# Performance work log

Measured on AMD Instinct MI355X. Metric: run time of the kernel, lower is better.

Reference implementation:

```python
import jax, jax.numpy as jnp
import numpy as np

B, N, C, NPOINT, NSAMPLE, NHEAD, NLAYERS, DOUT = 8, 4096, 128, 1024, 32, 4, 2, 256
EPS = 1e-5


def setup_inputs() -> dict:
    key = jax.random.key(0)
    ks = jax.random.split(key, 12)
    rn = lambda k, s: jax.random.normal(k, s, jnp.float32) * 0.05
    return {
        "xyz": jax.random.normal(ks[0], (B, 3, N), jnp.float32),
        "features": jax.random.normal(ks[1], (B, C, N), jnp.float32),
        # position-encoding MLP (1x1 convs) + BatchNorm2d (inference, running mean=0 var=1)
        "pe_w1": rn(ks[2], (C // 2, 3)), "pe_b1": jnp.zeros((C // 2,), jnp.float32),
        "bn_g": jnp.ones((C // 2,), jnp.float32), "bn_b": jnp.zeros((C // 2,), jnp.float32),
        "pe_w2": rn(ks[3], (C, C // 2)), "pe_b2": jnp.zeros((C,), jnp.float32),
        # 2 pre-norm transformer encoder layers (stacked params)
        "in_w": rn(ks[4], (NLAYERS, 3 * C, C)), "in_b": jnp.zeros((NLAYERS, 3 * C), jnp.float32),
        "out_w": rn(ks[5], (NLAYERS, C, C)), "out_b": jnp.zeros((NLAYERS, C), jnp.float32),
        "ln1_g": jnp.ones((NLAYERS, C), jnp.float32), "ln1_b": jnp.zeros((NLAYERS, C), jnp.float32),
        "ln2_g": jnp.ones((NLAYERS, C), jnp.float32), "ln2_b": jnp.zeros((NLAYERS, C), jnp.float32),
        "ff1_w": rn(ks[6], (NLAYERS, 2 * C, C)), "ff1_b": jnp.zeros((NLAYERS, 2 * C), jnp.float32),
        "ff2_w": rn(ks[7], (NLAYERS, C, 2 * C)), "ff2_b": jnp.zeros((NLAYERS, C), jnp.float32),
        # final 1x1 conv (fc)
        "fc_w": rn(ks[8], (DOUT, C)), "fc_b": jnp.zeros((DOUT,), jnp.float32),
    }


def _fps(pts, npoint):
    # pts: [B, N, 3]; iterative farthest point sampling (start at index 0)
    b, n, _ = pts.shape
    d0 = jnp.full((b, n), 1e10, pts.dtype)
    f0 = jnp.zeros((b,), jnp.int32)

    def step(carry, _):
        dist, far = carry
        c = jnp.take_along_axis(pts, far[:, None, None], axis=1)  # [B,1,3]
        d = jnp.sum((pts - c) ** 2, axis=-1)                      # [B,N]
        dist = jnp.minimum(dist, d)
        return (dist, jnp.argmax(dist, axis=-1).astype(jnp.int32)), far

    _, idx = jax.lax.scan(step, (d0, f0), None, length=npoint)
    return idx.T  # [B, npoint]


def _knn(nsample, pts, queries):
    # pts [B,N,3], queries [B,S,3] -> [B,S,nsample] nearest-neighbor indices
    sqd = (jnp.sum(queries ** 2, -1)[:, :, None] + jnp.sum(pts ** 2, -1)[:, None, :]
           - 2.0 * jnp.einsum('bsc,bnc->bsn', queries, pts))
    _, idx = jax.lax.top_k(-sqd, nsample)
    return idx


_gather = jax.vmap(lambda p, i: p[i])  # per-batch fancy gather


def _ln(x, g, b):
    m = jnp.mean(x, -1, keepdims=True)
    v = jnp.var(x, -1, keepdims=True)
    return (x - m) * jax.lax.rsqrt(v + EPS) * g + b


def _forward(xyz, features, pe_w1, pe_b1, bn_g, bn_b, pe_w2, pe_b2,
             in_w, in_b, out_w, out_b, ln1_g, ln1_b, ln2_g, ln2_b,
             ff1_w, ff1_b, ff2_w, ff2_b, fc_w, fc_b):
    xyz_t = xyz.transpose(0, 2, 1)                      # [B,N,3]
    fps_idx = _fps(xyz_t, NPOINT)                       # [B,S]
    new_xyz = _gather(xyz_t, fps_idx)                   # [B,S,3]
    gidx = _knn(NSAMPLE, xyz_t, new_xyz)                # [B,S,ns]
    gxyz = _gather(xyz_t, gidx)                         # [B,S,ns,3]
    gfeat = _gather(features.transpose(0, 2, 1), gidx)  # [B,S,ns,C]

    # position encoding: 1x1 conv MLP, BN in inference mode (mean=0, var=1)
    h = gxyz @ pe_w1.T + pe_b1
    h = h / jnp.sqrt(jnp.float32(1.0 + EPS)) * bn_g + bn_b
    pe = jax.nn.relu(h) @ pe_w2.T + pe_b2               # [B,S,ns,C]

    x = (gfeat + pe).reshape(B * NPOINT, NSAMPLE, C)    # groups as batch, seq=ns
    hd = C // NHEAD
    scale = 1.0 / jnp.sqrt(jnp.float32(hd))
    for l in range(NLAYERS):
        hN = _ln(x, ln1_g[l], ln1_b[l])
        qkv = hN @ in_w[l].T + in_b[l]
        q, k, v = jnp.split(qkv, 3, axis=-1)
        q = q.reshape(-1, NSAMPLE, NHEAD, hd)
        k = k.reshape(-1, NSAMPLE, NHEAD, hd)
        v = v.reshape(-1, NSAMPLE, NHEAD, hd)
        att = jax.nn.softmax(jnp.einsum('mqhd,mkhd->mhqk', q, k) * scale, axis=-1)
        a = jnp.einsum('mhqk,mkhd->mqhd', att, v).reshape(-1, NSAMPLE, C)
        x = x + (a @ out_w[l].T + out_b[l])
        h2 = _ln(x, ln2_g[l], ln2_b[l])
        x = x + (jax.nn.relu(h2 @ ff1_w[l].T + ff1_b[l]) @ ff2_w[l].T + ff2_b[l])

    pooled = x.reshape(B, NPOINT, NSAMPLE, C).max(axis=2)  # maxpool over neighbors
    out = pooled @ fc_w.T + fc_b                           # [B,S,DOUT]
    return new_xyz.transpose(0, 2, 1), out.transpose(0, 2, 1)


def reference(xyz, features, pe_w1, pe_b1, bn_g, bn_b, pe_w2, pe_b2,
              in_w, in_b, out_w, out_b, ln1_g, ln1_b, ln2_g, ln2_b,
              ff1_w, ff1_b, ff2_w, ff2_b, fc_w, fc_b):
    return _forward(xyz, features, pe_w1, pe_b1, bn_g, bn_b, pe_w2, pe_b2,
                    in_w, in_b, out_w, out_b, ln1_g, ln1_b, ln2_g, ln2_b,
                    ff1_w, ff1_b, ff2_w, ff2_b, fc_w, fc_b)
```

## Files before the change

### kernel.cpp

```cpp
#include <hip/hip_runtime.h>

typedef unsigned int u32;
typedef unsigned long long u64;
typedef unsigned short u16;
typedef __attribute__((ext_vector_type(8))) short bf16x8;
typedef __attribute__((ext_vector_type(4))) float f32x4;

#define DEV __device__ __forceinline__

DEV float sq3(float x, float y, float z) {
#pragma clang fp contract(off)
  return (x * x + y * y) + z * z;
}
DEV float knn_sqd(float4 Q, float4 p) {
#pragma clang fp contract(off)
  float dot = (Q.x * p.x + Q.y * p.y) + Q.z * p.z;
  return (Q.w + p.w) - 2.0f * dot;
}
DEV float dot4(float4 a, float4 b) {
  return (a.x * b.x + a.y * b.y) + (a.z * b.z + a.w * b.w);
}
DEV u32 f2bfu(float f) {
  u32 u = __float_as_uint(f);
  return (u + 0x7fffu + ((u >> 16) & 1u)) >> 16;
}
DEV f32x4 MFMA(bf16x8 a, bf16x8 b, f32x4 c) {
  return __builtin_amdgcn_mfma_f32_16x16x32_bf16(a, b, c, 0, 0, 0);
}

enum : int {
  W_PEW1 = 0, W_PEB1 = 192, W_BNG = 256, W_BNB = 320,
  W_PEW2 = 384, W_PEB2 = 8576,
  W_INW  = 8704,   W_INB  = 107008,
  W_OUTW = 107776, W_OUTB = 140544,
  W_LN1G = 140800, W_LN1B = 141056, W_LN2G = 141312, W_LN2B = 141568,
  W_FF1W = 141824, W_FF1B = 207360,
  W_FF2W = 207872, W_FF2B = 273408,
  W_FCW  = 273664, W_FCB  = 306432,
  W_TOTAL = 306688
};
enum : int { WP_QB = 0, WP_FB = 768, WP_TOTAL = 1280 };
enum : int {
  WB_Q  = 0,
  WB_O  = 98304,
  WB_F1 = 131072,
  WB_F2 = 196608,
  WB_P2 = 262144,
  WB_TOTAL = 270336
};

static const size_t OFF_XYZW  = 1226752;
static const size_t OFF_NEWX  = 1751040;
static const size_t OFF_KNN   = 1882112;
static const size_t OFF_WP    = 2930688;
static const size_t OFF_WB    = 2936064;
static const size_t OFF_FEATT = 3476736;
static const size_t END_BIG   = 20253952;

struct WArgs { const float* p[20]; };

__global__ void k_setup(WArgs a, float* __restrict__ wf, float* __restrict__ wp,
                        u16* __restrict__ wb, const float* __restrict__ xyz,
                        float4* __restrict__ xyzw) {
  const int blk = blockIdx.x, tid = threadIdx.x;
  if (blk < 1198) {
    const int idx = blk * 256 + tid;
    if (idx >= W_TOTAL) return;
    const int sz[20] = {192, 64, 64, 64, 8192, 128, 98304, 768, 32768, 256,
                        256, 256, 256, 256, 65536, 512, 65536, 256, 32768, 256};
    int rem = idx;
#pragma unroll
    for (int s = 0; s < 20; ++s) {
      if (rem < sz[s]) { wf[idx] = a.p[s][rem]; return; }
      rem -= sz[s];
    }
    return;
  }
  if (blk < 1206) {
    const int idx = (blk - 1198) * 256 + tid;
    if (idx >= 1920) return;
    if (idx < 768) {
      const int l = idx / 384, o = idx % 384;
      const float* W = a.p[6] + l * 49152 + o * 128;
      const float* G = a.p[10] + l * 128;
      const float* Bl = a.p[11] + l * 128;
      float acc = a.p[7][l * 384 + o];
      u16* ph = wb + WB_Q + (l * 384 + o) * 128;
      for (int c = 0; c < 128; ++c) {
        const float w = W[c];
        acc += Bl[c] * w;
        ph[c] = (u16)f2bfu(w * G[c]);
      }
      wp[WP_QB + l * 384 + o] = acc;
    } else if (idx < 1280) {
      const int j2 = idx - 768, l = j2 / 256, o = j2 % 256;
      const float* W = a.p[14] + l * 32768 + o * 128;
      const float* G = a.p[12] + l * 128;
      const float* Bl = a.p[13] + l * 128;
      float acc = a.p[15][l * 256 + o];
      u16* ph = wb + WB_F1 + (l * 256 + o) * 128;
      for (int c = 0; c < 128; ++c) {
        const float w = W[c];
        acc += Bl[c] * w;
        ph[c] = (u16)f2bfu(w * G[c]);
      }
      wp[WP_FB + l * 256 + o] = acc;
    } else if (idx < 1536) {
      const int j2 = idx - 1280, l = j2 / 128, o = j2 % 128;
      const float* W = a.p[8] + l * 16384 + o * 128;
      u16* ph = wb + WB_O + (l * 128 + o) * 128;
      for (int c = 0; c < 128; ++c) ph[c] = (u16)f2bfu(W[c]);
    } else if (idx < 1792) {
      const int j2 = idx - 1536, l = j2 / 128, o = j2 % 128;
      const float* W = a.p[16] + l * 32768 + o * 256;
      u16* ph = wb + WB_F2 + (l * 128 + o) * 256;
      for (int c = 0; c < 256; ++c) ph[c] = (u16)f2bfu(W[c]);
    } else {
      const int o = idx - 1792;
      const float* W = a.p[4] + o * 64;
      u16* ph = wb + WB_P2 + o * 64;
      for (int c = 0; c < 64; ++c) ph[c] = (u16)f2bfu(W[c]);
    }
    return;
  }
  {
    const int i = (blk - 1206) * 256 + tid;
    const int b = i >> 12, n = i & 4095;
    const size_t s = (size_t)b * 12288 + n;
    float x = xyz[s], y = xyz[s + 4096], z = xyz[s + 8192];
    xyzw[i] = make_float4(x, y, z, sq3(x, y, z));
  }
}

__global__ __launch_bounds__(256, 1) void k_pre(
    const float4* __restrict__ xyzw, float4* __restrict__ new_xyzw,
    float* __restrict__ out_xyz, const float* __restrict__ feat,
    float* __restrict__ featT) {
  __shared__ float PXs[4096], PYs[4096], PZs[4096];
  __shared__ u64 wkk[2][4];
  __shared__ float tile[32][33];
  const int tid = threadIdx.x;
  if (blockIdx.x >= 8) {
    const int bb = blockIdx.x - 8;
    const int b = bb >> 9, r2 = bb & 511;
    const int n0 = (r2 >> 2) << 5, c0 = (r2 & 3) << 5;
    const int tx = tid & 31, ty = tid >> 5;
#pragma unroll
    for (int i = 0; i < 4; ++i) {
      const int c = c0 + ty + (i << 3);
      tile[ty + (i << 3)][tx] =
          __builtin_nontemporal_load(&feat[(size_t)b * 524288 + (size_t)c * 4096 + n0 + tx]);
    }
    __syncthreads();
#pragma unroll
    for (int i = 0; i < 4; ++i) {
      const int n = n0 + ty + (i << 3);
      __builtin_nontemporal_store(tile[tx][ty + (i << 3)],
          &featT[(size_t)b * 524288 + (size_t)n * 128 + c0 + tx]);
    }
    return;
  }
  const int b = blockIdx.x;
  const float4* src = xyzw + (size_t)b * 4096;
  float px[16], py[16], pz[16], dm[16];
#pragma unroll
  for (int j = 0; j < 16; ++j) {
    float4 v = src[tid * 16 + j];
    PXs[tid * 16 + j] = v.x; PYs[tid * 16 + j] = v.y; PZs[tid * 16 + j] = v.z;
    px[j] = v.x; py[j] = v.y; pz[j] = v.z; dm[j] = 1e10f;
  }
  __syncthreads();
  float cx = PXs[0], cy = PYs[0], cz = PZs[0];
  if (tid == 0) {
    new_xyzw[(size_t)b * 1024] = make_float4(cx, cy, cz, sq3(cx, cy, cz));
    out_xyz[b * 3072]        = cx;
    out_xyz[b * 3072 + 1024] = cy;
    out_xyz[b * 3072 + 2048] = cz;
  }
  for (int t = 1; t < 1024; ++t) {
    {
      float dx = px[0] - cx, dy = py[0] - cy, dz = pz[0] - cz;
      dm[0] = fminf(dm[0], sq3(dx, dy, dz));
    }
    float bv = dm[0];
    int bi = tid * 16;
#pragma unroll
    for (int j = 1; j < 16; ++j) {
      float dx = px[j] - cx, dy = py[j] - cy, dz = pz[j] - cz;
      float d = sq3(dx, dy, dz);
      dm[j] = fminf(dm[j], d);
      if (dm[j] > bv) { bv = dm[j]; bi = tid * 16 + j; }
    }
    float mx = bv;
    mx = fmaxf(mx, __shfl_xor(mx, 1));
    mx = fmaxf(mx, __shfl_xor(mx, 2));
    mx = fmaxf(mx, __shfl_xor(mx, 4));
    mx = fmaxf(mx, __shfl_xor(mx, 8));
    mx = fmaxf(mx, __shfl_xor(mx, 16));
    mx = fmaxf(mx, __shfl_xor(mx, 32));
    const u64 ball = __ballot(bv == mx);
    const int wl2 = (int)(__ffsll((unsigned long long)ball) - 1);
    const int wbi = __shfl(bi, wl2);
    if ((tid & 63) == 0)
      wkk[t & 1][tid >> 6] = ((u64)__float_as_uint(mx) << 12) | (u32)(4095 - wbi);
    __syncthreads();
    const u64* wk = wkk[t & 1];
    u64 ka = wk[0] > wk[1] ? wk[0] : wk[1];
    u64 kb2 = wk[2] > wk[3] ? wk[2] : wk[3];
    u64 key = ka > kb2 ? ka : kb2;
    const int win = 4095 - (int)(key & 0xfffu);
    cx = PXs[win]; cy = PYs[win]; cz = PZs[win];
    if (tid == 0) {
      new_xyzw[(size_t)b * 1024 + t] = make_float4(cx, cy, cz, sq3(cx, cy, cz));
      out_xyz[b * 3072 + t]        = cx;
      out_xyz[b * 3072 + 1024 + t] = cy;
      out_xyz[b * 3072 + 2048 + t] = cz;
    }
  }
}

__global__ __launch_bounds__(128, 1) void k_knn(
    const float4* __restrict__ xyzw, const float4* __restrict__ qxyzw,
    int* __restrict__ knn) {
  __shared__ u64 LL[32 * 128];
  __shared__ int HH[4][32];
  const int tid = threadIdx.x;
  const int ql = tid >> 5, ss = tid & 31;
  const int b = blockIdx.x >> 8;
  const int q = ((blockIdx.x & 255) << 2) + ql;
  const float4 Q = qxyzw[(size_t)b * 1024 + q];
  u64 L[32];
#pragma unroll
  for (int i = 0; i < 32; ++i) L[i] = ~0ULL;
  const float4* P = xyzw + (size_t)b * 4096;
#pragma unroll 2
  for (int j = 0; j < 128; ++j) {
    const int n = j * 32 + ss;
    float4 p = P[n];
    float sqd = knn_sqd(Q, p);
    u32 u = __float_as_uint(sqd);
    u ^= (u32)((int)u >> 31) | 0x80000000u;
    const u64 key = ((u64)u << 12) | (u32)n;
    if (key < L[31]) {
#pragma unroll
      for (int i = 31; i >= 1; --i) {
        const u64 lo = L[i] < key ? L[i] : key;
        L[i] = lo > L[i - 1] ? lo : L[i - 1];
      }
      L[0] = L[0] < key ? L[0] : key;
    }
  }
#pragma unroll
  for (int i = 0; i < 32; ++i) LL[i * 128 + tid] = L[i];
  __syncthreads();
  if (ss == 0) {
#pragma unroll
    for (int t2 = 0; t2 < 32; ++t2) HH[ql][t2] = 0;
    const size_t ob = ((size_t)b * 1024 + q) * 32;
    for (int o = 0; o < 32; ++o) {
      u64 best = ~0ULL;
      int bs = 0;
#pragma unroll
      for (int t2 = 0; t2 < 32; ++t2) {
        const int hh = HH[ql][t2];
        const u64 v = (hh < 32) ? LL[hh * 128 + (ql * 32 + t2)] : ~0ULL;
        if (v < best) { best = v; bs = t2; }
      }
      HH[ql][bs]++;
      knn[ob + o] = (int)(best & 0xfffu);
    }
  }
}


DEV void ln_z(const float* __restrict__ X, u16* __restrict__ ZH, int tid) {
  const int r = tid >> 3, sub = tid & 7;
  const int xm = (r & 7) << 2;
  const float* row = X + r * 128;
  float4 v[4];
  float s = 0.f;
#pragma unroll
  for (int j = 0; j < 4; ++j) {
    v[j] = *(const float4*)&row[(sub * 16 + j * 4) ^ xm];
    s += (v[j].x + v[j].y) + (v[j].z + v[j].w);
  }
  s += __shfl_xor(s, 1); s += __shfl_xor(s, 2); s += __shfl_xor(s, 4);
  const float m = s * 0.0078125f;
  float qv = 0.f;
#pragma unroll
  for (int j = 0; j < 4; ++j) {
    float a = v[j].x - m, b = v[j].y - m, c = v[j].z - m, d = v[j].w - m;
    qv += (a * a + b * b) + (c * c + d * d);
  }
  qv += __shfl_xor(qv, 1); qv += __shfl_xor(qv, 2); qv += __shfl_xor(qv, 4);
  const float rstd = 1.0f / sqrtf(qv * 0.0078125f + 1e-5f);
  const int mask = (r & 7) << 3;
  float z[16];
#pragma unroll
  for (int j = 0; j < 4; ++j) {
    z[j * 4]     = (v[j].x - m) * rstd;
    z[j * 4 + 1] = (v[j].y - m) * rstd;
    z[j * 4 + 2] = (v[j].z - m) * rstd;
    z[j * 4 + 3] = (v[j].w - m) * rstd;
  }
#pragma unroll
  for (int i = 0; i < 8; ++i) {
    const u32 w = f2bfu(z[2 * i]) | (f2bfu(z[2 * i + 1]) << 16);
    *(u32*)&ZH[r * 128 + ((sub * 16 + 2 * i) ^ mask)] = w;
  }
}

template <int K, int AINS, int MODE>
DEV void gemmT(const u16* __restrict__ A, const u16* __restrict__ wbp,
               const float* __restrict__ bias, float* __restrict__ X,
               u16* __restrict__ OUTp, int co, int tid) {
  const int wv = tid >> 6, wl = tid & 63;
  const int c0 = wv * 32;
  const int lm = wl & 15, kb = wl >> 4;
  const int amask = (lm & 7) << 3;
  constexpr int KS = K / 32;
  constexpr int CH = (KS > 4) ? 4 : KS;
  f32x4 acc[2][2];
#pragma unroll
  for (int m = 0; m < 2; ++m)
#pragma unroll
    for (int t = 0; t < 2; ++t) acc[m][t] = (f32x4){0.f, 0.f, 0.f, 0.f};
#pragma unroll
  for (int kc = 0; kc < KS / CH; ++kc) {
    bf16x8 bfr[CH][2];
#pragma unroll
    for (int ks = 0; ks < CH; ++ks) {
      const int k0 = (kc * CH + ks) * 32 + kb * 8;
#pragma unroll
      for (int t = 0; t < 2; ++t)
        bfr[ks][t] = *(const bf16x8*)&wbp[(size_t)(c0 + t * 16 + lm) * K + k0];
    }
#pragma unroll
    for (int ks = 0; ks < CH; ++ks) {
      const int k0 = (kc * CH + ks) * 32 + kb * 8;
      const bf16x8 a0 = *(const bf16x8*)&A[(size_t)lm * AINS + (k0 ^ amask)];
      const bf16x8 a1 = *(const bf16x8*)&A[(size_t)(16 + lm) * AINS + (k0 ^ amask)];
#pragma unroll
      for (int t = 0; t < 2; ++t) {
        acc[0][t] = MFMA(a0, bfr[ks][t], acc[0][t]);
        acc[1][t] = MFMA(a1, bfr[ks][t], acc[1][t]);
      }
    }
  }
#pragma unroll
  for (int m = 0; m < 2; ++m)
#pragma unroll
    for (int t = 0; t < 2; ++t) {
      const int col = c0 + t * 16 + lm;
      const float bv = bias[col];
      if (MODE == 3) {
        const int j0 = m * 16 + kb * 4;
        const int base = (col & 31) * 256 + 128 + ((col >> 5) << 5) +
                         (j0 ^ ((col & 3) << 3));
        *(u32*)&OUTp[base]     = f2bfu(acc[m][t][0] + bv) | (f2bfu(acc[m][t][1] + bv) << 16);
        *(u32*)&OUTp[base + 2] = f2bfu(acc[m][t][2] + bv) | (f2bfu(acc[m][t][3] + bv) << 16);
      } else if (MODE == 1) {
#pragma unroll
        for (int j = 0; j < 4; ++j) {
          const int row = m * 16 + kb * 4 + j;
          X[row * 128 + (col ^ ((row & 7) << 2))] += acc[m][t][j] + bv;
        }
      } else {
#pragma unroll
        for (int j = 0; j < 4; ++j) {
          const int row = m * 16 + kb * 4 + j;
          float val = acc[m][t][j] + bv;
          if (MODE == 2) val = fmaxf(val, 0.f);
          OUTp[row * 256 + ((co + col) ^ ((row & 7) << 3))] = (u16)f2bfu(val);
        }
      }
    }
}

__global__ __launch_bounds__(256, 2) void k_xform(
    const float* __restrict__ feat, const float* __restrict__ featT, const int useT,
    const float4* __restrict__ xyzw, const int* __restrict__ knn,
    const float* __restrict__ wf, const float* __restrict__ wp,
    const u16* __restrict__ wb, float* __restrict__ out) {
  __shared__ __align__(16) float sm[10240];
  float* X  = sm;
  u16* ZH   = (u16*)(sm + 4096);
  u16* QKp  = (u16*)(sm + 6144);
  const int g = blockIdx.x, b = g >> 10, tid = threadIdx.x;
  const int r = tid >> 3, sub = tid & 7, cs = sub * 16;
  const int xm = (r & 7) << 2;
  const int n = knn[g * 32 + r];
  if (useT) {
    const f32x4* srcp = (const f32x4*)(featT + ((size_t)(b * 4096 + n)) * 128 + cs);
    float* dst = &X[r * 128];
#pragma unroll
    for (int j = 0; j < 4; ++j)
      *(f32x4*)&dst[(cs + j * 4) ^ xm] = __builtin_nontemporal_load(&srcp[j]);
  } else {
    const size_t fb0 = (size_t)b * 524288 + n;
    float* dst = &X[r * 128];
#pragma unroll
    for (int j = 0; j < 16; ++j)
      dst[(cs + j) ^ xm] = __builtin_nontemporal_load(&feat[fb0 + (size_t)(cs + j) * 4096]);
  }
  {
    const float4 g4 = xyzw[(size_t)b * 4096 + n];
    const float rs = 1.0f / sqrtf(1.0f + 1e-5f);
    const int mask = (r & 7) << 3;
#pragma unroll
    for (int i = 0; i < 4; ++i) {
      u32 wpk = 0;
#pragma unroll
      for (int e = 0; e < 2; ++e) {
        const int c = sub * 8 + 2 * i + e;
        float hv = g4.x * wf[W_PEW1 + c * 3] + g4.y * wf[W_PEW1 + c * 3 + 1] +
                   g4.z * wf[W_PEW1 + c * 3 + 2] + wf[W_PEB1 + c];
        hv = hv * (wf[W_BNG + c] * rs) + wf[W_BNB + c];
        hv = fmaxf(hv, 0.f);
        wpk |= f2bfu(hv) << (16 * e);
      }
      *(u32*)&ZH[r * 128 + ((sub * 8 + 2 * i) ^ mask)] = wpk;
    }
  }
  __syncthreads();
  gemmT<64, 128, 1>(ZH, wb + WB_P2, wf + W_PEB2, X, QKp, 0, tid);
  __syncthreads();
#pragma unroll 1
  for (int l = 0; l < 2; ++l) {
    ln_z(X, ZH, tid);
    __syncthreads();
    gemmT<128, 128, 0>(ZH, wb + WB_Q + l * 49152, wp + WP_QB + l * 384,
                       X, QKp, 0, tid);
    gemmT<128, 128, 0>(ZH, wb + WB_Q + l * 49152 + 16384,
                       wp + WP_QB + l * 384 + 128, X, QKp, 128, tid);
    __syncthreads();
    {
      const int wv = tid >> 6, wl = tid & 63;
      const int hh = wv, lm = wl & 15, kb = wl >> 4;
      bf16x8 qf[2], kf[2];
#pragma unroll
      for (int t = 0; t < 2; ++t) {
        const int rr = t * 16 + lm;
        const int msk = (rr & 7) << 3;
        qf[t] = *(const bf16x8*)&QKp[rr * 256 + ((hh * 32 + kb * 8) ^ msk)];
        kf[t] = *(const bf16x8*)&QKp[rr * 256 + ((128 + hh * 32 + kb * 8) ^ msk)];
      }
      __syncthreads();
      const f32x4 zz = {0.f, 0.f, 0.f, 0.f};
      f32x4 sc[2][2];
      sc[0][0] = MFMA(qf[0], kf[0], zz); sc[0][1] = MFMA(qf[0], kf[1], zz);
      sc[1][0] = MFMA(qf[1], kf[0], zz); sc[1][1] = MFMA(qf[1], kf[1], zz);
      const float scale = 0.1767766952966369f;
      u16* Pw = QKp + hh * 32;
#pragma unroll
      for (int mtl = 0; mtl < 2; ++mtl) {
#pragma unroll
        for (int j = 0; j < 4; ++j) {
          float a0 = sc[mtl][0][j] * scale, a1 = sc[mtl][1][j] * scale;
          float mx = fmaxf(a0, a1);
          mx = fmaxf(mx, __shfl_xor(mx, 1));
          mx = fmaxf(mx, __shfl_xor(mx, 2));
          mx = fmaxf(mx, __shfl_xor(mx, 4));
          mx = fmaxf(mx, __shfl_xor(mx, 8));
          const float e0 = __expf(a0 - mx), e1 = __expf(a1 - mx);
          float sum = e0 + e1;
          sum += __shfl_xor(sum, 1); sum += __shfl_xor(sum, 2);
          sum += __shfl_xor(sum, 4); sum += __shfl_xor(sum, 8);
          const float inv = 1.0f / sum;
          const int q2 = mtl * 16 + kb * 4 + j;
          const int qm = (q2 & 3) << 3;
          Pw[q2 * 256 + (lm ^ qm)]        = (u16)f2bfu(e0 * inv);
          Pw[q2 * 256 + ((16 + lm) ^ qm)] = (u16)f2bfu(e1 * inv);
        }
      }
    }
    __syncthreads();
    gemmT<128, 128, 3>(ZH, wb + WB_Q + l * 49152 + 32768,
                       wp + WP_QB + l * 384 + 256, X, QKp, 0, tid);
    __syncthreads();
    {
      const int wv = tid >> 6, wl = tid & 63;
      const int hh = wv, lm = wl & 15, kb = wl >> 4;
      const f32x4 zz = {0.f, 0.f, 0.f, 0.f};
      bf16x8 pf[2], vf[2];
#pragma unroll
      for (int t = 0; t < 2; ++t) {
        const int q2 = t * 16 + lm;
        pf[t] = *(const bf16x8*)&QKp[q2 * 256 + hh * 32 +
                                     ((kb * 8) ^ ((q2 & 3) << 3))];
        const int d = hh * 32 + t * 16 + lm;
        vf[t] = *(const bf16x8*)&QKp[(d & 31) * 256 + 128 + hh * 32 +
                                     ((kb * 8) ^ ((d & 3) << 3))];
      }
      f32x4 av[2][2];
      av[0][0] = MFMA(pf[0], vf[0], zz); av[0][1] = MFMA(pf[0], vf[1], zz);
      av[1][0] = MFMA(pf[1], vf[0], zz); av[1][1] = MFMA(pf[1], vf[1], zz);
#pragma unroll
      for (int mtl = 0; mtl < 2; ++mtl)
#pragma unroll
        for (int ntl = 0; ntl < 2; ++ntl)
#pragma unroll
          for (int j = 0; j < 4; ++j) {
            const int row = mtl * 16 + kb * 4 + j;
            const int col = hh * 32 + ntl * 16 + lm;
            ZH[row * 128 + (col ^ ((row & 7) << 3))] = (u16)f2bfu(av[mtl][ntl][j]);
          }
    }
    __syncthreads();
    gemmT<128, 128, 1>(ZH, wb + WB_O + l * 16384, wf + W_OUTB + l * 128,
                       X, QKp, 0, tid);
    __syncthreads();
    ln_z(X, ZH, tid);
    __syncthreads();
    gemmT<128, 128, 2>(ZH, wb + WB_F1 + l * 32768, wp + WP_FB + l * 256,
                       X, QKp, 0, tid);
    gemmT<128, 128, 2>(ZH, wb + WB_F1 + l * 32768 + 16384,
                       wp + WP_FB + l * 256 + 128, X, QKp, 128, tid);
    __syncthreads();
    gemmT<256, 256, 1>(QKp, wb + WB_F2 + l * 32768, wf + W_FF2B + l * 128,
                       X, QKp, 0, tid);
    __syncthreads();
  }
  float* pooled = (float*)ZH;
  if (tid < 128) {
    float m = X[(tid ^ 0)];
#pragma unroll
    for (int rr = 1; rr < 32; ++rr)
      m = fmaxf(m, X[rr * 128 + (tid ^ ((rr & 7) << 2))]);
    pooled[tid] = m;
  }
  __syncthreads();
  {
    float acc = wf[W_FCB + tid];
    const float* wr = wf + W_FCW + tid * 128;
#pragma unroll 8
    for (int c = 0; c < 128; c += 4) {
      float4 w4 = *(const float4*)&wr[c];
      float4 x4 = *(const float4*)&pooled[c];
      acc += dot4(x4, w4);
    }
    const int s = g & 1023;
    __builtin_nontemporal_store(acc,
        &out[24576 + (size_t)b * 262144 + (size_t)tid * 1024 + s]);
  }
}

extern "C" void kernel_launch(void* const* d_in, const int* in_sizes, int n_in,
                              void* d_out, int out_size, void* d_ws, size_t ws_size,
                              hipStream_t stream) {
  (void)in_sizes; (void)n_in; (void)out_size;
  char* ws = (char*)d_ws;
  float* wf    = (float*)ws;
  float4* xyzw = (float4*)(ws + OFF_XYZW);
  float4* newx = (float4*)(ws + OFF_NEWX);
  int* knni    = (int*)(ws + OFF_KNN);
  float* wp    = (float*)(ws + OFF_WP);
  u16* wb      = (u16*)(ws + OFF_WB);
  const float* xyz  = (const float*)d_in[0];
  const float* feat = (const float*)d_in[1];
  const int useT = (ws_size >= END_BIG) ? 1 : 0;
  float* featT = useT ? (float*)(ws + OFF_FEATT) : (float*)d_in[1];
  WArgs wa;
  for (int i = 0; i < 20; ++i) wa.p[i] = (const float*)d_in[2 + i];
  float* outp = (float*)d_out;

  hipLaunchKernelGGL(k_setup, dim3(1334), dim3(256), 0, stream, wa, wf, wp, wb, xyz, xyzw);
  hipLaunchKernelGGL(k_pre, dim3(useT ? 4104 : 8), dim3(256), 0, stream,
                     xyzw, newx, outp, feat, featT);
  hipLaunchKernelGGL(k_knn, dim3(2048), dim3(128), 0, stream, xyzw, newx, knni);
  hipLaunchKernelGGL(k_xform, dim3(8192), dim3(256), 0, stream,
                     feat, featT, useT, xyzw, knni, wf, wp, wb, outp);
}
```

Before: 2.134 ms.

## Process two query groups per block to reuse weight fragments across 64 rows

Result: faster. 2.015 ms (-5.5%).

```diff
diff --git a/kernel.cpp b/kernel.cpp
--- a/kernel.cpp
+++ b/kernel.cpp
@@ -320,9 +320,9 @@
   const int amask = (lm & 7) << 3;
   constexpr int KS = K / 32;
   constexpr int CH = (KS > 4) ? 4 : KS;
-  f32x4 acc[2][2];
-#pragma unroll
-  for (int m = 0; m < 2; ++m)
+  f32x4 acc[4][2];
+#pragma unroll
+  for (int m = 0; m < 4; ++m)
 #pragma unroll
     for (int t = 0; t < 2; ++t) acc[m][t] = (f32x4){0.f, 0.f, 0.f, 0.f};
 #pragma unroll
@@ -338,25 +338,27 @@
 #pragma unroll
     for (int ks = 0; ks < CH; ++ks) {
       const int k0 = (kc * CH + ks) * 32 + kb * 8;
-      const bf16x8 a0 = *(const bf16x8*)&A[(size_t)lm * AINS + (k0 ^ amask)];
-      const bf16x8 a1 = *(const bf16x8*)&A[(size_t)(16 + lm) * AINS + (k0 ^ amask)];
-#pragma unroll
-      for (int t = 0; t < 2; ++t) {
-        acc[0][t] = MFMA(a0, bfr[ks][t], acc[0][t]);
-        acc[1][t] = MFMA(a1, bfr[ks][t], acc[1][t]);
-      }
-    }
-  }
-#pragma unroll
-  for (int m = 0; m < 2; ++m)
+      bf16x8 a[4];
+#pragma unroll
+      for (int m = 0; m < 4; ++m)
+        a[m] = *(const bf16x8*)&A[(size_t)(m * 16 + lm) * AINS + (k0 ^ amask)];
+#pragma unroll
+      for (int m = 0; m < 4; ++m)
+#pragma unroll
+        for (int t = 0; t < 2; ++t)
+          acc[m][t] = MFMA(a[m], bfr[ks][t], acc[m][t]);
+    }
+  }
+#pragma unroll
+  for (int m = 0; m < 4; ++m)
 #pragma unroll
     for (int t = 0; t < 2; ++t) {
       const int col = c0 + t * 16 + lm;
       const float bv = bias[col];
       if (MODE == 3) {
-        const int j0 = m * 16 + kb * 4;
-        const int base = (col & 31) * 256 + 128 + ((col >> 5) << 5) +
-                         (j0 ^ ((col & 3) << 3));
+        const int j0 = (m & 1) * 16 + kb * 4;
+        const int base = (m >> 1) * 8192 + (col & 31) * 256 + 128 +
+                         ((col >> 5) << 5) + (j0 ^ ((col & 3) << 3));
         *(u32*)&OUTp[base]     = f2bfu(acc[m][t][0] + bv) | (f2bfu(acc[m][t][1] + bv) << 16);
         *(u32*)&OUTp[base + 2] = f2bfu(acc[m][t][2] + bv) | (f2bfu(acc[m][t][3] + bv) << 16);
       } else if (MODE == 1) {
@@ -382,28 +384,28 @@
     const float4* __restrict__ xyzw, const int* __restrict__ knn,
     const float* __restrict__ wf, const float* __restrict__ wp,
     const u16* __restrict__ wb, float* __restrict__ out) {
-  __shared__ __align__(16) float sm[10240];
+  __shared__ __align__(16) float sm[20480];
   float* X  = sm;
-  u16* ZH   = (u16*)(sm + 4096);
-  u16* QKp  = (u16*)(sm + 6144);
-  const int g = blockIdx.x, b = g >> 10, tid = threadIdx.x;
+  u16* ZH   = (u16*)(sm + 8192);
+  u16* QKp  = (u16*)(sm + 12288);
+  const int g0 = blockIdx.x * 2, b = g0 >> 10, tid = threadIdx.x;
   const int r = tid >> 3, sub = tid & 7, cs = sub * 16;
   const int xm = (r & 7) << 2;
-  const int n = knn[g * 32 + r];
-  if (useT) {
-    const f32x4* srcp = (const f32x4*)(featT + ((size_t)(b * 4096 + n)) * 128 + cs);
-    float* dst = &X[r * 128];
-#pragma unroll
-    for (int j = 0; j < 4; ++j)
-      *(f32x4*)&dst[(cs + j * 4) ^ xm] = __builtin_nontemporal_load(&srcp[j]);
-  } else {
-    const size_t fb0 = (size_t)b * 524288 + n;
-    float* dst = &X[r * 128];
-#pragma unroll
-    for (int j = 0; j < 16; ++j)
-      dst[(cs + j) ^ xm] = __builtin_nontemporal_load(&feat[fb0 + (size_t)(cs + j) * 4096]);
-  }
-  {
+#pragma unroll
+  for (int grp = 0; grp < 2; ++grp) {
+    const int n = knn[(g0 + grp) * 32 + r];
+    float* dst = &X[(grp * 32 + r) * 128];
+    if (useT) {
+      const f32x4* srcp = (const f32x4*)(featT + ((size_t)(b * 4096 + n)) * 128 + cs);
+#pragma unroll
+      for (int j = 0; j < 4; ++j)
+        *(f32x4*)&dst[(cs + j * 4) ^ xm] = __builtin_nontemporal_load(&srcp[j]);
+    } else {
+      const size_t fb0 = (size_t)b * 524288 + n;
+#pragma unroll
+      for (int j = 0; j < 16; ++j)
+        dst[(cs + j) ^ xm] = __builtin_nontemporal_load(&feat[fb0 + (size_t)(cs + j) * 4096]);
+    }
     const float4 g4 = xyzw[(size_t)b * 4096 + n];
     const float rs = 1.0f / sqrtf(1.0f + 1e-5f);
     const int mask = (r & 7) << 3;
@@ -419,7 +421,7 @@
         hv = fmaxf(hv, 0.f);
         wpk |= f2bfu(hv) << (16 * e);
       }
-      *(u32*)&ZH[r * 128 + ((sub * 8 + 2 * i) ^ mask)] = wpk;
+      *(u32*)&ZH[(grp * 32 + r) * 128 + ((sub * 8 + 2 * i) ^ mask)] = wpk;
     }
   }
   __syncthreads();
@@ -428,6 +430,7 @@
 #pragma unroll 1
   for (int l = 0; l < 2; ++l) {
     ln_z(X, ZH, tid);
+    ln_z(X + 4096, ZH + 4096, tid);
     __syncthreads();
     gemmT<128, 128, 0>(ZH, wb + WB_Q + l * 49152, wp + WP_QB + l * 384,
                        X, QKp, 0, tid);
@@ -437,40 +440,49 @@
     {
       const int wv = tid >> 6, wl = tid & 63;
       const int hh = wv, lm = wl & 15, kb = wl >> 4;
-      bf16x8 qf[2], kf[2];
-#pragma unroll
-      for (int t = 0; t < 2; ++t) {
-        const int rr = t * 16 + lm;
-        const int msk = (rr & 7) << 3;
-        qf[t] = *(const bf16x8*)&QKp[rr * 256 + ((hh * 32 + kb * 8) ^ msk)];
-        kf[t] = *(const bf16x8*)&QKp[rr * 256 + ((128 + hh * 32 + kb * 8) ^ msk)];
+      bf16x8 qf[2][2], kf[2][2];
+#pragma unroll
+      for (int grp = 0; grp < 2; ++grp) {
+        const u16* Qb = QKp + grp * 8192;
+#pragma unroll
+        for (int t = 0; t < 2; ++t) {
+          const int rr = t * 16 + lm;
+          const int msk = (rr & 7) << 3;
+          qf[grp][t] = *(const bf16x8*)&Qb[rr * 256 + ((hh * 32 + kb * 8) ^ msk)];
+          kf[grp][t] = *(const bf16x8*)&Qb[rr * 256 + ((128 + hh * 32 + kb * 8) ^ msk)];
+        }
       }
       __syncthreads();
+      const float scale = 0.1767766952966369f;
       const f32x4 zz = {0.f, 0.f, 0.f, 0.f};
-      f32x4 sc[2][2];
-      sc[0][0] = MFMA(qf[0], kf[0], zz); sc[0][1] = MFMA(qf[0], kf[1], zz);
-      sc[1][0] = MFMA(qf[1], kf[0], zz); sc[1][1] = MFMA(qf[1], kf[1], zz);
-      const float scale = 0.1767766952966369f;
-      u16* Pw = QKp + hh * 32;
-#pragma unroll
-      for (int mtl = 0; mtl < 2; ++mtl) {
-#pragma unroll
-        for (int j = 0; j < 4; ++j) {
-          float a0 = sc[mtl][0][j] * scale, a1 = sc[mtl][1][j] * scale;
-          float mx = fmaxf(a0, a1);
-          mx = fmaxf(mx, __shfl_xor(mx, 1));
-          mx = fmaxf(mx, __shfl_xor(mx, 2));
-          mx = fmaxf(mx, __shfl_xor(mx, 4));
-          mx = fmaxf(mx, __shfl_xor(mx, 8));
-          const float e0 = __expf(a0 - mx), e1 = __expf(a1 - mx);
-          float sum = e0 + e1;
-          sum += __shfl_xor(sum, 1); sum += __shfl_xor(sum, 2);
-          sum += __shfl_xor(sum, 4); sum += __shfl_xor(sum, 8);
-          const float inv = 1.0f / sum;
-          const int q2 = mtl * 16 + kb * 4 + j;
-          const int qm = (q2 & 3) << 3;
-          Pw[q2 * 256 + (lm ^ qm)]        = (u16)f2bfu(e0 * inv);
-          Pw[q2 * 256 + ((16 + lm) ^ qm)] = (u16)f2bfu(e1 * inv);
+#pragma unroll
+      for (int grp = 0; grp < 2; ++grp) {
+        f32x4 sc[2][2];
+        sc[0][0] = MFMA(qf[grp][0], kf[grp][0], zz);
+        sc[0][1] = MFMA(qf[grp][0], kf[grp][1], zz);
+        sc[1][0] = MFMA(qf[grp][1], kf[grp][0], zz);
+        sc[1][1] = MFMA(qf[grp][1], kf[grp][1], zz);
+        u16* Pw = QKp + grp * 8192 + hh * 32;
+#pragma unroll
+        for (int mtl = 0; mtl < 2; ++mtl) {
+#pragma unroll
+          for (int j = 0; j < 4; ++j) {
+            float a0 = sc[mtl][0][j] * scale, a1 = sc[mtl][1][j] * scale;
+            float mx = fmaxf(a0, a1);
+            mx = fmaxf(mx, __shfl_xor(mx, 1));
+            mx = fmaxf(mx, __shfl_xor(mx, 2));
+            mx = fmaxf(mx, __shfl_xor(mx, 4));
+            mx = fmaxf(mx, __shfl_xor(mx, 8));
+            const float e0 = __expf(a0 - mx), e1 = __expf(a1 - mx);
+            float sum = e0 + e1;
+            sum += __shfl_xor(sum, 1); sum += __shfl_xor(sum, 2);
+            sum += __shfl_xor(sum, 4); sum += __shfl_xor(sum, 8);
+            const float inv = 1.0f / sum;
+            const int q2 = mtl * 16 + kb * 4 + j;
+            const int qm = (q2 & 3) << 3;
+            Pw[q2 * 256 + (lm ^ qm)]        = (u16)f2bfu(e0 * inv);
+            Pw[q2 * 256 + ((16 + lm) ^ qm)] = (u16)f2bfu(e1 * inv);
+          }
         }
       }
     }
@@ -482,35 +494,41 @@
       const int wv = tid >> 6, wl = tid & 63;
       const int hh = wv, lm = wl & 15, kb = wl >> 4;
       const f32x4 zz = {0.f, 0.f, 0.f, 0.f};
-      bf16x8 pf[2], vf[2];
-#pragma unroll
-      for (int t = 0; t < 2; ++t) {
-        const int q2 = t * 16 + lm;
-        pf[t] = *(const bf16x8*)&QKp[q2 * 256 + hh * 32 +
-                                     ((kb * 8) ^ ((q2 & 3) << 3))];
-        const int d = hh * 32 + t * 16 + lm;
-        vf[t] = *(const bf16x8*)&QKp[(d & 31) * 256 + 128 + hh * 32 +
-                                     ((kb * 8) ^ ((d & 3) << 3))];
-      }
-      f32x4 av[2][2];
-      av[0][0] = MFMA(pf[0], vf[0], zz); av[0][1] = MFMA(pf[0], vf[1], zz);
-      av[1][0] = MFMA(pf[1], vf[0], zz); av[1][1] = MFMA(pf[1], vf[1], zz);
-#pragma unroll
-      for (int mtl = 0; mtl < 2; ++mtl)
-#pragma unroll
-        for (int ntl = 0; ntl < 2; ++ntl)
-#pragma unroll
-          for (int j = 0; j < 4; ++j) {
-            const int row = mtl * 16 + kb * 4 + j;
-            const int col = hh * 32 + ntl * 16 + lm;
-            ZH[row * 128 + (col ^ ((row & 7) << 3))] = (u16)f2bfu(av[mtl][ntl][j]);
-          }
+#pragma unroll
+      for (int grp = 0; grp < 2; ++grp) {
+        const u16* Qb = QKp + grp * 8192;
+        bf16x8 pf[2], vf[2];
+#pragma unroll
+        for (int t = 0; t < 2; ++t) {
+          const int q2 = t * 16 + lm;
+          pf[t] = *(const bf16x8*)&Qb[q2 * 256 + hh * 32 +
+                                      ((kb * 8) ^ ((q2 & 3) << 3))];
+          const int d = hh * 32 + t * 16 + lm;
+          vf[t] = *(const bf16x8*)&Qb[(d & 31) * 256 + 128 + hh * 32 +
+                                      ((kb * 8) ^ ((d & 3) << 3))];
+        }
+        f32x4 av[2][2];
+        av[0][0] = MFMA(pf[0], vf[0], zz); av[0][1] = MFMA(pf[0], vf[1], zz);
+        av[1][0] = MFMA(pf[1], vf[0], zz); av[1][1] = MFMA(pf[1], vf[1], zz);
+#pragma unroll
+        for (int mtl = 0; mtl < 2; ++mtl)
+#pragma unroll
+          for (int ntl = 0; ntl < 2; ++ntl)
+#pragma unroll
+            for (int j = 0; j < 4; ++j) {
+              const int row = mtl * 16 + kb * 4 + j;
+              const int col = hh * 32 + ntl * 16 + lm;
+              ZH[(grp * 32 + row) * 128 + (col ^ ((row & 7) << 3))] =
+                  (u16)f2bfu(av[mtl][ntl][j]);
+            }
+      }
     }
     __syncthreads();
     gemmT<128, 128, 1>(ZH, wb + WB_O + l * 16384, wf + W_OUTB + l * 128,
                        X, QKp, 0, tid);
     __syncthreads();
     ln_z(X, ZH, tid);
+    ln_z(X + 4096, ZH + 4096, tid);
     __syncthreads();
     gemmT<128, 128, 2>(ZH, wb + WB_F1 + l * 32768, wp + WP_FB + l * 256,
                        X, QKp, 0, tid);
@@ -523,25 +541,34 @@
   }
   float* pooled = (float*)ZH;
   if (tid < 128) {
-    float m = X[(tid ^ 0)];
-#pragma unroll
-    for (int rr = 1; rr < 32; ++rr)
-      m = fmaxf(m, X[rr * 128 + (tid ^ ((rr & 7) << 2))]);
-    pooled[tid] = m;
+#pragma unroll
+    for (int grp = 0; grp < 2; ++grp) {
+      const float* Xg = X + grp * 4096;
+      float m = Xg[tid];
+#pragma unroll
+      for (int rr = 1; rr < 32; ++rr)
+        m = fmaxf(m, Xg[rr * 128 + (tid ^ ((rr & 7) << 2))]);
+      pooled[grp * 128 + tid] = m;
+    }
   }
   __syncthreads();
   {
-    float acc = wf[W_FCB + tid];
     const float* wr = wf + W_FCW + tid * 128;
+    const float bias = wf[W_FCB + tid];
+#pragma unroll
+    for (int grp = 0; grp < 2; ++grp) {
+      float acc = bias;
+      const float* pg = pooled + grp * 128;
 #pragma unroll 8
-    for (int c = 0; c < 128; c += 4) {
-      float4 w4 = *(const float4*)&wr[c];
-      float4 x4 = *(const float4*)&pooled[c];
-      acc += dot4(x4, w4);
-    }
-    const int s = g & 1023;
-    __builtin_nontemporal_store(acc,
-        &out[24576 + (size_t)b * 262144 + (size_t)tid * 1024 + s]);
+      for (int c = 0; c < 128; c += 4) {
+        float4 w4 = *(const float4*)&wr[c];
+        float4 x4 = *(const float4*)&pg[c];
+        acc += dot4(x4, w4);
+      }
+      const int s = (g0 + grp) & 1023;
+      __builtin_nontemporal_store(acc,
+          &out[24576 + (size_t)b * 262144 + (size_t)tid * 1024 + s]);
+    }
   }
 }
 
@@ -568,6 +595,6 @@
   hipLaunchKernelGGL(k_pre, dim3(useT ? 4104 : 8), dim3(256), 0, stream,
                      xyzw, newx, outp, feat, featT);
   hipLaunchKernelGGL(k_knn, dim3(2048), dim3(128), 0, stream, xyzw, newx, knni);
-  hipLaunchKernelGGL(k_xform, dim3(8192), dim3(256), 0, stream,
+  hipLaunchKernelGGL(k_xform, dim3(4096), dim3(256), 0, stream,
                      feat, featT, useT, xyzw, knni, wf, wp, wb, outp);
 }
```
